# Optimization experiments

Hardware: AMD Instinct MI355X
Metric: run time of the kernel (lower is better)

## Reference

```python
import math
import jax, jax.numpy as jnp
import numpy as np

N_NODES = 100000
N_EDGES = 1200000
N_BASIS = 20
HIDDEN = 50
SILU_NORM = 1.679  # e3nn normalize2mom constant for silu
LMAX_SH = 5
MID_LS = (0, 1, 2, 3, 4)          # middle = 1x0e+1x1o+1x2e+1x3o+1x4e (dim 25)
OUT_L = 2                          # out = 1x2e (dim 5)
TP2_PATHS = ((0, 2), (1, 1), (1, 3), (2, 0), (2, 2), (2, 4), (3, 1), (3, 3), (3, 5), (4, 2), (4, 4))
NUM_NEIGHBORS = 6


def _fact(n):
    return math.factorial(n)


def _cg(j1, m1, j2, m2, j3, m3):
    # Racah formula for Clebsch-Gordan coefficients (complex SH, Condon-Shortley).
    if m1 + m2 != m3:
        return 0.0
    pref = math.sqrt((2 * j3 + 1) * _fact(j1 + j2 - j3) * _fact(j1 - j2 + j3) * _fact(-j1 + j2 + j3) / _fact(j1 + j2 + j3 + 1))
    pref *= math.sqrt(_fact(j1 + m1) * _fact(j1 - m1) * _fact(j2 + m2) * _fact(j2 - m2) * _fact(j3 + m3) * _fact(j3 - m3))
    s = 0.0
    for k in range(j1 + j2 - j3 + 1):
        d = (k, j1 + j2 - j3 - k, j1 - m1 - k, j2 + m2 - k, j3 - j2 + m1 + k, j3 - j1 - m2 + k)
        if min(d) < 0:
            continue
        den = 1.0
        for q in d:
            den *= _fact(q)
        s += (-1.0) ** k / den
    return pref * s


def _u_real(l):
    # change of basis complex SH -> real SH, rows indexed by real m=-l..l
    U = np.zeros((2 * l + 1, 2 * l + 1), dtype=np.complex128)
    U[l, l] = 1.0
    rt2 = math.sqrt(2.0)
    for m in range(1, l + 1):
        U[l + m, l + m] = (-1.0) ** m / rt2
        U[l + m, l - m] = 1.0 / rt2
        U[l - m, l + m] = -1j * (-1.0) ** m / rt2
        U[l - m, l - m] = 1j / rt2
    return U


def _w3j_real(j1, j2, j3):
    # real-basis Wigner 3j tensor (real for even j1+j2+j3, which holds for all paths here)
    Wc = np.zeros((2 * j1 + 1, 2 * j2 + 1, 2 * j3 + 1), dtype=np.complex128)
    for m1 in range(-j1, j1 + 1):
        for m2 in range(-j2, j2 + 1):
            m3 = -(m1 + m2)
            if abs(m3) <= j3:
                Wc[j1 + m1, j2 + m2, j3 + m3] = (-1.0) ** (j1 - j2 - m3) / math.sqrt(2 * j3 + 1) * _cg(j1, m1, j2, m2, j3, -m3)
    U1, U2, U3 = _u_real(j1).conj(), _u_real(j2).conj(), _u_real(j3).conj()
    Wr = np.einsum('abc,ia,jb,kc->ijk', Wc, U1, U2, U3)
    return np.ascontiguousarray(Wr.real.astype(np.float32))


W3J_TP1 = {l: _w3j_real(0, l, l) for l in MID_LS}
W3J_TP2 = {p: _w3j_real(p[0], p[1], OUT_L) for p in TP2_PATHS}


def spherical_harmonics(vec):
    # vec [E,3] -> component-normalized real SH for l=0..5, concatenated [E,36]
    r = jnp.sqrt(jnp.sum(vec * vec, axis=1))
    x, y, z = vec[:, 0] / r, vec[:, 1] / r, vec[:, 2] / r
    phi = jnp.arctan2(y, x)
    s = jnp.sqrt(jnp.clip(1.0 - z * z, 0.0, 1.0))
    # associated Legendre P[l][m] without Condon-Shortley phase
    P = [[None] * (l + 1) for l in range(LMAX_SH + 1)]
    P[0][0] = jnp.ones_like(z)
    for m in range(1, LMAX_SH + 1):
        P[m][m] = (2 * m - 1) * s * P[m - 1][m - 1]
    for m in range(0, LMAX_SH):
        P[m + 1][m] = (2 * m + 1) * z * P[m][m]
    for l in range(2, LMAX_SH + 1):
        for m in range(0, l - 1):
            P[l][m] = ((2 * l - 1) * z * P[l - 1][m] - (l - 1 + m) * P[l - 2][m]) / (l - m)
    blocks = []
    for l in range(LMAX_SH + 1):
        comps = []
        for m in range(-l, l + 1):
            am = abs(m)
            c = math.sqrt((2 * l + 1) * _fact(l - am) / _fact(l + am)) * (math.sqrt(2.0) if m != 0 else 1.0)
            if m < 0:
                ang = jnp.sin(am * phi)
            elif m > 0:
                ang = jnp.cos(am * phi)
            else:
                ang = jnp.ones_like(phi)
            comps.append(c * P[l][am] * ang)
        blocks.append(jnp.stack(comps, axis=1))
    return jnp.concatenate(blocks, axis=1)


def soft_one_hot(d):
    # e3nn soft_one_hot_linspace(basis='smooth_finite', cutoff=True), start=0, end=3
    values = jnp.linspace(0.0, 3.0, N_BASIS + 2)
    step = values[1] - values[0]
    values = values[1:-1]
    diff = (d[:, None] - values[None, :]) / step

    def sus(t):
        safe = jnp.where(t > 0, t, 1.0)
        return jnp.where(t > 0, jnp.exp(-1.0 / safe), 0.0)

    return 1.14136 * math.exp(2.0) * sus(diff + 1.0) * sus(1.0 - diff)


def tp1(x_scalar, sh, w):
    # FullyConnectedTensorProduct(1x0e, sh, middle) with external per-edge weights w [E,5]
    outs = []
    for i, l in enumerate(MID_LS):
        W = W3J_TP1[l][0]                       # [2l+1, 2l+1]
        alpha = math.sqrt(2 * l + 1)            # sqrt(dim_out / fan_in), fan_in = 1
        shl = sh[:, l * l:(l + 1) * (l + 1)]
        outs.append(alpha * w[:, i:i + 1] * x_scalar * (shl @ W))
    return jnp.concatenate(outs, axis=1)        # [E, 25]


def tp2(feat, sh, w):
    # FullyConnectedTensorProduct(middle, sh, 1x2e) with internal weights w [11]
    alpha = math.sqrt((2 * OUT_L + 1) / len(TP2_PATHS))
    out = jnp.zeros((feat.shape[0], 2 * OUT_L + 1), dtype=feat.dtype)
    for p, (l1, l2) in enumerate(TP2_PATHS):
        W = W3J_TP2[(l1, l2)]                   # [2l1+1, 2l2+1, 5]
        f = feat[:, l1 * l1:(l1 + 1) * (l1 + 1)]
        s = sh[:, l2 * l2:(l2 + 1) * (l2 + 1)]
        tmp = jnp.einsum('ei,ijk->ejk', f, W)
        out = out + (alpha * w[p]) * jnp.einsum('ejk,ej->ek', tmp, s)
    return out                                   # [E, 5]


def _forward(x, pos, edge_index, mlp_w1, mlp_w2, tp2_w):
    N = pos.shape[0]
    edge_from = edge_index[:, 0]
    edge_to = edge_index[:, 1]
    Co = jnp.argmax(jnp.bincount(edge_to, length=N))          # torch.mode(edge_to)
    edge_vec = pos[edge_to] - pos[edge_from]
    sh = spherical_harmonics(edge_vec)                         # [E, 36]
    dist = jnp.linalg.norm(edge_vec, axis=1)
    emb = soft_one_hot(dist)                                   # [E, 20]
    h = jax.nn.silu(emb @ mlp_w1 / math.sqrt(N_BASIS)) * SILU_NORM
    tp_w = h @ mlp_w2 / math.sqrt(HIDDEN)                      # [E, 5]
    feat = tp1(x[edge_to], sh, tp_w)                           # [E, 25]
    node = jax.ops.segment_sum(feat, edge_from, num_segments=N) / math.sqrt(float(NUM_NEIGHBORS))
    feat2 = tp2(node[edge_to], sh, tp2_w)                      # [E, 5]
    node2 = jax.ops.segment_sum(feat2, edge_from, num_segments=N)
    return node2[Co]                                           # [5]


def setup_inputs():
    N, E = N_NODES, N_EDGES
    key = jax.random.key(0)
    k = jax.random.split(key, 7)
    pos = 1.5 * jax.random.normal(k[0], (N, 3), dtype=jnp.float32)
    x = jax.random.normal(k[1], (N, 1), dtype=jnp.float32)
    ef = jax.random.randint(k[2], (E,), 0, N, dtype=jnp.int32)
    off = jax.random.randint(k[3], (E,), 1, N, dtype=jnp.int32)
    et = (ef + off) % N                                        # no self loops -> nonzero edge_vec
    edge_index = jnp.stack([ef, et], axis=1)
    mlp_w1 = jax.random.normal(k[4], (N_BASIS, HIDDEN), dtype=jnp.float32)
    mlp_w2 = jax.random.normal(k[5], (HIDDEN, len(MID_LS)), dtype=jnp.float32)
    tp2_w = jax.random.normal(k[6], (len(TP2_PATHS),), dtype=jnp.float32)
    return {'x': x, 'pos': pos, 'edge_index': edge_index, 'mlp_w1': mlp_w1, 'mlp_w2': mlp_w2, 'tp2_w': tp2_w}


def reference(x, pos, edge_index, mlp_w1, mlp_w2, tp2_w):
    return _forward(x, pos, edge_index, mlp_w1, mlp_w2, tp2_w)
```

## Files before the change

kernel.cpp:

```cpp
#include <hip/hip_runtime.h>
#include <math.h>

#define CAP 2048
#define HALF_MAX 12544


struct WSPtrs {
  unsigned* slices;
  int* flag;
  unsigned long long* key;
  int* co_count;
  int* s_count;
  int* co_edges;
  float* node_acc;
  float* w3j1;
  float* w3j2;
  size_t fb_zero_bytes;
  size_t total_bytes;
};

__host__ __device__ inline WSPtrs make_ws(char* ws, int N, int half, int C, int fb){
  WSPtrs p;
  size_t o = 0;
  p.slices   = (unsigned*)(ws + o);
  o += fb ? (size_t)N * 4 : (size_t)C * 2 * half * 4;
  p.flag     = (int*)(ws + o); o += (size_t)N * 4;
  o = (o + 7) & ~(size_t)7;
  p.key      = (unsigned long long*)(ws + o); o += 8;
  p.co_count = (int*)(ws + o); o += 4;
  p.s_count  = (int*)(ws + o); o += 4;
  p.co_edges = (int*)(ws + o); o += (size_t)CAP * 4;
  p.node_acc = (float*)(ws + o); o += (size_t)CAP * 25 * 4;
  p.fb_zero_bytes = o;
  p.w3j1     = (float*)(ws + o); o += 165 * 4;
  p.w3j2     = (float*)(ws + o); o += 1915 * 4;
  p.total_bytes = o;
  return p;
}


__device__ double cg_coef_lut(int j1,int m1,int j2,int m2,int j3,int m3, const double* __restrict__ fact){
  if (m1 + m2 != m3) return 0.0;
  double pref = sqrt((2.0*j3+1.0) * fact[j1+j2-j3] * fact[j1-j2+j3] * fact[-j1+j2+j3]
                     / fact[j1+j2+j3+1]);
  pref *= sqrt(fact[j1+m1]*fact[j1-m1]*fact[j2+m2]*fact[j2-m2]*fact[j3+m3]*fact[j3-m3]);
  double s = 0.0;
  for (int k = 0; k <= j1+j2-j3; ++k){
    int d2 = j1-m1-k, d3 = j2+m2-k, d4 = j3-j2+m1+k, d5 = j3-j1-m2+k;
    if (d2 < 0 || d3 < 0 || d4 < 0 || d5 < 0) continue;
    double den = fact[k]*fact[j1+j2-j3-k]*fact[d2]*fact[d3]*fact[d4]*fact[d5];
    s += ((k & 1) ? -1.0 : 1.0) / den;
  }
  return pref * s;
}

__device__ double wigner_c_val_lut(int j1,int j2,int j3,int m1,int m2,int m3, const double* __restrict__ fact){
  if (m1+m2+m3 != 0) return 0.0;
  int e = j1 - j2 - m3;
  double sign = (e & 1) ? -1.0 : 1.0;
  return sign / sqrt(2.0*j3+1.0) * cg_coef_lut(j1,m1,j2,m2,j3,-m3,fact);
}

__device__ int conjU_row(int l, int i, int* cols, double* re, double* im){
  int mr = i - l;
  const double irt2 = 0.70710678118654752440;
  if (mr == 0){ cols[0]=l; re[0]=1.0; im[0]=0.0; return 1; }
  int m = mr > 0 ? mr : -mr;
  double sgn = (m & 1) ? -1.0 : 1.0;
  if (mr > 0){
    cols[0]=l+m; re[0]=sgn*irt2; im[0]=0.0;
    cols[1]=l-m; re[1]=irt2;     im[1]=0.0;
  } else {
    cols[0]=l+m; re[0]=0.0; im[0]= sgn*irt2;
    cols[1]=l-m; re[1]=0.0; im[1]=-irt2;
  }
  return 2;
}

__device__ void wigner_entry(int entry, const double* __restrict__ sfact,
                             float* __restrict__ w3j1, float* __restrict__ w3j2){
  if (entry >= 165 + 1915) return;
  int j1, j2, j3, ii, jj, kk;
  float* dst;
  if (entry < 165){
    const int l1off[5] = {0,1,10,35,84};
    int l = 4;
    for (int q = 1; q < 5; ++q) if (entry < l1off[q]){ l = q-1; break; }
    int t = entry - l1off[l];
    int n = 2*l+1;
    j1 = 0; j2 = l; j3 = l;
    ii = 0; jj = t / n; kk = t % n;
    dst = &w3j1[entry];
  } else {
    int t2 = entry - 165;
    const int pl1[11]  = {0,1,1,2,2,2,3,3,3,4,4};
    const int pl2[11]  = {2,1,3,0,2,4,1,3,5,2,4};
    const int poff[11] = {0,25,70,175,200,325,550,655,900,1285,1510};
    int p = 10;
    for (int q = 1; q < 11; ++q) if (t2 < poff[q]){ p = q-1; break; }
    int t = t2 - poff[p];
    j1 = pl1[p]; j2 = pl2[p]; j3 = 2;
    int n2q = 2*j2+1;
    ii = t / (n2q*5); int rem = t % (n2q*5); jj = rem / 5; kk = rem % 5;
    dst = &w3j2[t2];
  }
  int c1[2], c2[2], c3[2];
  double r1[2], i1[2], r2[2], i2[2], r3[2], i3[2];
  int n1 = conjU_row(j1, ii, c1, r1, i1);
  int n2 = conjU_row(j2, jj, c2, r2, i2);
  int n3 = conjU_row(j3, kk, c3, r3, i3);
  double acc = 0.0;
  for (int combo = 0; combo < 8; ++combo){
    int a = (combo >> 2) & 1, b = (combo >> 1) & 1, c = combo & 1;
    if (a >= n1 || b >= n2 || c >= n3) continue;
    int m1 = c1[a]-j1, m2 = c2[b]-j2, m3 = c3[c]-j3;
    if (m1 + m2 + m3 != 0) continue;
    double wc = wigner_c_val_lut(j1,j2,j3,m1,m2,m3,sfact);
    if (wc == 0.0) continue;
    double pr = r1[a]*r2[b] - i1[a]*i2[b];
    double pi = r1[a]*i2[b] + i1[a]*r2[b];
    acc += wc * (pr*r3[c] - pi*i3[c]);
  }
  *dst = (float)acc;
}


__device__ void compute_sh36f(float ex, float ey, float ez, float* __restrict__ sh){
  float r = sqrtf(ex*ex + ey*ey + ez*ez);
  float x = ex/r, y = ey/r, z = ez/r;
  float t = 1.0f - z*z;
  t = t < 0.0f ? 0.0f : (t > 1.0f ? 1.0f : t);
  float s = sqrtf(t);
  float rxy = sqrtf(x*x + y*y);
  float c1, s1;
  if (rxy > 1e-30f){ c1 = x/rxy; s1 = y/rxy; } else { c1 = 1.0f; s1 = 0.0f; }
  float cm[6], sm[6];
  cm[0] = 1.0f; sm[0] = 0.0f;
  for (int m = 1; m <= 5; ++m){
    cm[m] = cm[m-1]*c1 - sm[m-1]*s1;
    sm[m] = sm[m-1]*c1 + cm[m-1]*s1;
  }
  float P[6][6];
  P[0][0] = 1.0f;
  for (int m=1;m<=5;m++) P[m][m] = (float)(2*m-1)*s*P[m-1][m-1];
  for (int m=0;m<5;m++)  P[m+1][m] = (float)(2*m+1)*z*P[m][m];
  for (int l=2;l<=5;l++)
    for (int m=0;m<=l-2;m++)
      P[l][m] = ((float)(2*l-1)*z*P[l-1][m] - (float)(l-1+m)*P[l-2][m])/(float)(l-m);
  const float rt2 = 1.41421356237309504880f;
  for (int l=0;l<=5;l++){
    for (int m=-l;m<=l;m++){
      int am = m < 0 ? -m : m;
      float ratio = 1.0f;
      for (int k = l-am+1; k <= l+am; ++k) ratio *= (float)k;
      float c = sqrtf((float)(2*l+1)/ratio);
      if (m != 0) c *= rt2;
      float ang = (m < 0) ? sm[am] : ((m > 0) ? cm[am] : 1.0f);
      sh[l*l + m + l] = c * P[l][am] * ang;
    }
  }
}

__device__ void feat_edge(int f, int t, const int* __restrict__ flag,
                          const float* __restrict__ pos, const float* __restrict__ x,
                          const float* w1, const float* w2,
                          const float* w3j1, float* __restrict__ node_acc){
  int slot = flag[f] - 1;
  if (slot < 0 || slot >= CAP) return;

  float ex = pos[3*t+0] - pos[3*f+0];
  float ey = pos[3*t+1] - pos[3*f+1];
  float ez = pos[3*t+2] - pos[3*f+2];
  float sh[36];
  compute_sh36f(ex,ey,ez,sh);
  float d = sqrtf(ex*ex+ey*ey+ez*ez);

  float emb[20];
  const float step = 3.0f/21.0f;
  const float cemb = 1.14136f * 7.38905609893065f;
  for (int jb=0;jb<20;jb++){
    float v = step*(float)(jb+1);
    float diff = (d - v)/step;
    float a = diff + 1.0f, b = 1.0f - diff;
    float sa = (a > 0.0f) ? __expf(-1.0f/a) : 0.0f;
    float sb = (b > 0.0f) ? __expf(-1.0f/b) : 0.0f;
    emb[jb] = cemb * sa * sb;
  }
  float tw[5] = {0,0,0,0,0};
  const float is20 = 0.22360679774997896964f;
  const float is50 = 0.14142135623730950488f;
  for (int kk=0;kk<50;kk++){
    float z = 0.0f;
    for (int jb=0;jb<20;jb++) z += emb[jb]*w1[jb*50+kk];
    z *= is20;
    float hk = (z / (1.0f + __expf(-z))) * 1.679f;
    for (int i=0;i<5;i++) tw[i] += hk * w2[kk*5+i];
  }
  for (int i=0;i<5;i++) tw[i] *= is50;

  float xs = x[t];
  const int w1off[5] = {0,1,10,35,84};
  const float alphal[5] = {1.0f, 1.73205080756887729353f, 2.23606797749978969641f,
                           2.64575131106459059050f, 3.0f};
  int fo = 0;
  for (int l=0;l<5;l++){
    int nl = 2*l+1;
    float scale = alphal[l] * tw[l] * xs;
    for (int kq=0;kq<nl;kq++){
      float acc = 0.0f;
      for (int jq=0;jq<nl;jq++) acc += sh[l*l+jq]*w3j1[w1off[l]+jq*nl+kq];
      atomicAdd(&node_acc[slot*25 + fo + kq], scale*acc);
    }
    fo += nl;
  }
}

__device__ void tp2_task(int e, int p, const int2* __restrict__ ei, const int* __restrict__ flag,
                         const float* __restrict__ pos, const float* __restrict__ node_acc,
                         const float* w3j2, const float* __restrict__ tp2w,
                         float* __restrict__ acc){
  const float inv_sqrt6 = 0.40824829046386301637f;
  const float alpha2    = 0.67419986246324704794f;
  const int pl1[11]  = {0,1,1,2,2,2,3,3,3,4,4};
  const int pl2[11]  = {2,1,3,0,2,4,1,3,5,2,4};
  const int poff[11] = {0,25,70,175,200,325,550,655,900,1285,1510};
  int2 fe = ei[e];
  int f = fe.x, t = fe.y;
  int slot = flag[t] - 1;
  if (slot < 0 || slot >= CAP) return;
  float ex = pos[3*t+0] - pos[3*f+0];
  float ey = pos[3*t+1] - pos[3*f+1];
  float ez = pos[3*t+2] - pos[3*f+2];
  float sh[36];
  compute_sh36f(ex,ey,ez,sh);
  int l1 = pl1[p], l2 = pl2[p], n1 = 2*l1+1, n2 = 2*l2+1;
  const float* W = w3j2 + poff[p];
  float wp = alpha2 * tp2w[p];
  for (int i=0;i<n1;i++){
    float fi = node_acc[slot*25 + l1*l1 + i] * inv_sqrt6;
    for (int j=0;j<n2;j++){
      float fs = wp*fi*sh[l2*l2+j];
      const float* Wij = W + (i*n2+j)*5;
      for (int k=0;k<5;k++) acc[k] += fs*Wij[k];
    }
  }
}


__global__ __launch_bounds__(1024)
void count_w3j_kernel(const int2* __restrict__ ei, unsigned* __restrict__ slices,
                      int* __restrict__ flag, unsigned long long* __restrict__ key,
                      int* __restrict__ co_count, int* __restrict__ s_count,
                      float* __restrict__ node_acc,
                      float* __restrict__ w3j1, float* __restrict__ w3j2,
                      int N, int half, int E, int C){
  __shared__ double sfact[16];
  __shared__ unsigned hist[HALF_MAX];
  if (threadIdx.x == 0){
    double rr = 1.0;
    sfact[0] = 1.0;
    for (int i = 1; i < 16; ++i){ rr *= (double)i; sfact[i] = rr; }
  }
  for (int i = threadIdx.x; i < half; i += blockDim.x) hist[i] = 0;
  __syncthreads();

  int gtid = blockIdx.x*blockDim.x + threadIdx.x;
  int gsize = gridDim.x*blockDim.x;

  if (gtid < 2080) wigner_entry(gtid, sfact, w3j1, w3j2);
  for (int i = gtid; i < N; i += gsize) flag[i] = 0;
  for (int i = gtid; i < CAP*25; i += gsize) node_acc[i] = 0.0f;
  if (gtid == 0){ *key = 0ull; *co_count = 0; *s_count = 0; }

  int c = blockIdx.x >> 1;
  int r = blockIdx.x & 1;
  int wbase = r * half;
  size_t e0 = (size_t)c * (size_t)E / (size_t)C;
  size_t e1 = (size_t)(c+1) * (size_t)E / (size_t)C;
  for (size_t e = e0 + threadIdx.x; e < e1; e += blockDim.x){
    int v = ei[e].y;
    int lw = (v >> 2) - wbase;
    if (lw >= 0 && lw < half)
      atomicAdd(&hist[lw], 1u << ((v & 3) * 8));
  }
  __syncthreads();

  unsigned* dst = slices + (size_t)(c*2 + r) * half;
  for (int i = threadIdx.x; i < half; i += blockDim.x) dst[i] = hist[i];
}

__global__ void count_fb_kernel(const int2* __restrict__ ei, unsigned* __restrict__ counts,
                                float* __restrict__ w3j1, float* __restrict__ w3j2, int E){
  __shared__ double sfact[16];
  if (threadIdx.x == 0){
    double rr = 1.0;
    sfact[0] = 1.0;
    for (int i = 1; i < 16; ++i){ rr *= (double)i; sfact[i] = rr; }
  }
  __syncthreads();
  int tid = blockIdx.x*blockDim.x + threadIdx.x;
  if (tid < 2080) wigner_entry(tid, sfact, w3j1, w3j2);
  if (tid < E) atomicAdd(&counts[ei[tid].y], 1u);
}

__global__ void argmax_kernel(const unsigned* __restrict__ slices, unsigned long long* __restrict__ key,
                              int N, int Nw, int half, int C, int fb){
  __shared__ unsigned long long sred[256];
  int w = blockIdx.x*blockDim.x + threadIdx.x;
  unsigned long long best = 0;
  if (fb){
    if (w < N)
      best = ((unsigned long long)slices[w] << 32) | (unsigned)(N-1-w);
  } else if (w < Nw){
    int r = (w >= half) ? 1 : 0;
    int lw = w - r*half;
    unsigned sum = 0;
    for (int c = 0; c < C; ++c)
      sum += slices[(size_t)(c*2 + r) * half + lw];
    for (int q = 0; q < 4; ++q){
      int idx = w*4 + q;
      if (idx < N){
        unsigned cnt = (sum >> (q*8)) & 0xffu;
        unsigned long long k = ((unsigned long long)cnt << 32) | (unsigned)(N-1-idx);
        if (k > best) best = k;
      }
    }
  }
  sred[threadIdx.x] = best;
  __syncthreads();
  for (int s = 128; s > 0; s >>= 1){
    if (threadIdx.x < s){
      unsigned long long o = sred[threadIdx.x+s];
      if (o > sred[threadIdx.x]) sred[threadIdx.x] = o;
    }
    __syncthreads();
  }
  if (threadIdx.x == 0) atomicMax(key, sred[0]);
}

__global__ void find_co_kernel(const int2* __restrict__ ei, const unsigned long long* __restrict__ key,
                               int* __restrict__ flag, int* __restrict__ co_count,
                               int* __restrict__ s_count, int* __restrict__ co_edges, int N, int E){
  int e = blockIdx.x*blockDim.x + threadIdx.x;
  if (e >= E) return;
  int Co = N - 1 - (int)(unsigned int)(*key & 0xffffffffull);
  int2 fe = ei[e];
  if (fe.x != Co) return;
  int p = atomicAdd(co_count, 1);
  if (p < CAP) co_edges[p] = e;
  int v = fe.y;
  if (atomicCAS(&flag[v], 0, -1) == 0){
    int slot = atomicAdd(s_count, 1);
    flag[v] = (slot < CAP) ? (slot + 1) : 0;
  }
}

__global__ void collect_feat_kernel(const int2* __restrict__ ei, const int* __restrict__ flag,
                                    const float* __restrict__ pos, const float* __restrict__ x,
                                    const float* __restrict__ w1g, const float* __restrict__ w2g,
                                    const float* __restrict__ w3j1g, float* __restrict__ node_acc,
                                    int E){
  __shared__ float sw1[1000];
  __shared__ float sw2[250];
  __shared__ float sw3j1[165];
  int e = blockIdx.x*blockDim.x + threadIdx.x;
  int2 fe = make_int2(0, 0);
  int has = 0;
  if (e < E){ fe = ei[e]; has = (flag[fe.x] > 0); }
  if (__syncthreads_or(has) == 0) return;

  for (int i = threadIdx.x; i < 1000; i += blockDim.x) sw1[i] = w1g[i];
  for (int i = threadIdx.x; i < 250;  i += blockDim.x) sw2[i] = w2g[i];
  for (int i = threadIdx.x; i < 165;  i += blockDim.x) sw3j1[i] = w3j1g[i];
  __syncthreads();
  if (!has) return;

  feat_edge(fe.x, fe.y, flag, pos, x, sw1, sw2, sw3j1, node_acc);
}

__global__ void out_kernel(const int2* __restrict__ ei, const int* __restrict__ flag,
                           const float* __restrict__ pos, const float* __restrict__ node_acc,
                           const float* __restrict__ w3j2g, const float* __restrict__ tp2w,
                           const int* __restrict__ co_count, const int* __restrict__ co_edges,
                           float* __restrict__ out){
  __shared__ float sw3j2[1915];
  __shared__ float red[256*5];
  for (int i = threadIdx.x; i < 1915; i += blockDim.x) sw3j2[i] = w3j2g[i];
  __syncthreads();
  float acc[5] = {0,0,0,0,0};
  int n = *co_count; if (n > CAP) n = CAP;
  int tasks = n * 11;
  for (int task = threadIdx.x; task < tasks; task += blockDim.x)
    tp2_task(co_edges[task/11], task%11, ei, flag, pos, node_acc, sw3j2, tp2w, acc);
  for (int k=0;k<5;k++) red[threadIdx.x*5+k] = acc[k];
  __syncthreads();
  if (threadIdx.x < 5){
    float s = 0.0f;
    for (int t2=0;t2<256;t2++) s += red[t2*5+threadIdx.x];
    out[threadIdx.x] = s;
  }
}


extern "C" void kernel_launch(void* const* d_in, const int* in_sizes, int n_in,
                              void* d_out, int out_size, void* d_ws, size_t ws_size,
                              hipStream_t stream){
  const int2*  ei2  = (const int2*)d_in[2];
  const float* xp   = (const float*)d_in[0];
  const float* posp = (const float*)d_in[1];
  const float* w1p  = (const float*)d_in[3];
  const float* w2p  = (const float*)d_in[4];
  const float* tpwp = (const float*)d_in[5];
  float* outp = (float*)d_out;
  char* wsp = (char*)d_ws;
  int N = in_sizes[0];
  int E = in_sizes[2] / 2;
  int Nw = (N + 3) >> 2;
  int half = (Nw + 1) >> 1;

  int fb = (half > HALF_MAX) ? 1 : 0;
  int C = 0;
  if (!fb){
    for (int cand = 128; cand >= 8; cand >>= 1){
      WSPtrs p = make_ws(wsp, N, half, cand, 0);
      if (p.total_bytes + 64 <= ws_size){ C = cand; break; }
    }
    if (C == 0) fb = 1;
  }
  WSPtrs P = make_ws(wsp, N, half, fb ? 1 : C, fb);

  int eblocks = (E + 255)/256;
  if (fb){
    hipMemsetAsync(d_ws, 0, P.fb_zero_bytes, stream);
    count_fb_kernel<<<eblocks, 256, 0, stream>>>(ei2, P.slices, P.w3j1, P.w3j2, E);
  } else {
    count_w3j_kernel<<<2*C, 1024, 0, stream>>>(ei2, P.slices, P.flag, P.key,
                                               P.co_count, P.s_count, P.node_acc,
                                               P.w3j1, P.w3j2, N, half, E, C);
  }
  int ablocks = fb ? (N + 255)/256 : (Nw + 255)/256;
  argmax_kernel     <<<ablocks, 256, 0, stream>>>(P.slices, P.key, N, Nw, half, C, fb);
  find_co_kernel    <<<eblocks, 256, 0, stream>>>(ei2, P.key, P.flag, P.co_count, P.s_count,
                                                  P.co_edges, N, E);
  collect_feat_kernel<<<eblocks, 256, 0, stream>>>(ei2, P.flag, posp, xp, w1p, w2p, P.w3j1,
                                                   P.node_acc, E);
  out_kernel        <<<1, 256, 0, stream>>>(ei2, P.flag, posp, P.node_acc, P.w3j2, tpwp,
                                            P.co_count, P.co_edges, outp);
}
```

Measured before the change: 166.7 us.

## Fuse argmax, center search, feature collect and output into one cooperative kernel

Measured after the change: 322.7 us. +93.6%, slower.

```diff
diff --git a/kernel.cpp b/kernel.cpp
--- a/kernel.cpp
+++ b/kernel.cpp
@@ -1,7 +1,11 @@
 #include <hip/hip_runtime.h>
+#include <hip/hip_cooperative_groups.h>
 #include <math.h>
 
+namespace cg = cooperative_groups;
+
 #define CAP 2048
+#define SLIST 64
 #define HALF_MAX 12544
 
 
@@ -11,6 +15,7 @@
   unsigned long long* key;
   int* co_count;
   int* s_count;
+  int* s_nodes;
   int* co_edges;
   float* node_acc;
   float* w3j1;
@@ -29,6 +34,7 @@
   p.key      = (unsigned long long*)(ws + o); o += 8;
   p.co_count = (int*)(ws + o); o += 4;
   p.s_count  = (int*)(ws + o); o += 4;
+  p.s_nodes  = (int*)(ws + o); o += SLIST * 4;
   p.co_edges = (int*)(ws + o); o += (size_t)CAP * 4;
   p.node_acc = (float*)(ws + o); o += (size_t)CAP * 25 * 4;
   p.fb_zero_bytes = o;
@@ -161,13 +167,11 @@
   }
 }
 
-__device__ void feat_edge(int f, int t, const int* __restrict__ flag,
-                          const float* __restrict__ pos, const float* __restrict__ x,
-                          const float* w1, const float* w2,
-                          const float* w3j1, float* __restrict__ node_acc){
-  int slot = flag[f] - 1;
+__device__ void feat_edge_slot(int f, int t, int slot,
+                               const float* __restrict__ pos, const float* __restrict__ x,
+                               const float* w1, const float* w2,
+                               const float* w3j1, float* __restrict__ node_acc){
   if (slot < 0 || slot >= CAP) return;
-
   float ex = pos[3*t+0] - pos[3*f+0];
   float ey = pos[3*t+1] - pos[3*f+1];
   float ez = pos[3*t+2] - pos[3*f+2];
@@ -303,6 +307,124 @@
   if (tid < E) atomicAdd(&counts[ei[tid].y], 1u);
 }
 
+
+__global__ void tail_kernel(const int2* __restrict__ ei, const float* __restrict__ pos,
+                            const float* __restrict__ x, const float* __restrict__ w1g,
+                            const float* __restrict__ w2g, const float* __restrict__ tp2w,
+                            char* __restrict__ ws, float* __restrict__ out,
+                            int N, int Nw, int half, int E, int C, int fb){
+  cg::grid_group grid = cg::this_grid();
+  WSPtrs P = make_ws(ws, N, half, fb ? 1 : C, fb);
+
+  __shared__ unsigned long long sred[256];
+  __shared__ float fred[256*5];
+  __shared__ float sw1[1000];
+  __shared__ float sw2[250];
+  __shared__ float sw3j1[165];
+  __shared__ float sw3j2[1915];
+  __shared__ int s_list[SLIST];
+
+  int tid = blockIdx.x*blockDim.x + threadIdx.x;
+  int nth = gridDim.x*blockDim.x;
+
+  {
+    unsigned long long best = 0;
+    if (fb){
+      const unsigned* counts = P.slices;
+      for (int i = tid; i < N; i += nth){
+        unsigned long long k = ((unsigned long long)counts[i] << 32) | (unsigned)(N-1-i);
+        if (k > best) best = k;
+      }
+    } else {
+      for (int w = tid; w < Nw; w += nth){
+        int r = (w >= half) ? 1 : 0;
+        int lw = w - r*half;
+        unsigned sum = 0;
+        for (int c = 0; c < C; ++c)
+          sum += P.slices[(size_t)(c*2 + r) * half + lw];
+        for (int q = 0; q < 4; ++q){
+          int idx = w*4 + q;
+          if (idx < N){
+            unsigned cnt = (sum >> (q*8)) & 0xffu;
+            unsigned long long k = ((unsigned long long)cnt << 32) | (unsigned)(N-1-idx);
+            if (k > best) best = k;
+          }
+        }
+      }
+    }
+    sred[threadIdx.x] = best;
+    __syncthreads();
+    for (int s = 128; s > 0; s >>= 1){
+      if (threadIdx.x < s){
+        unsigned long long o = sred[threadIdx.x+s];
+        if (o > sred[threadIdx.x]) sred[threadIdx.x] = o;
+      }
+      __syncthreads();
+    }
+    if (threadIdx.x == 0) atomicMax(P.key, sred[0]);
+  }
+  grid.sync();
+
+  {
+    int Co = N - 1 - (int)(unsigned int)(*P.key & 0xffffffffull);
+    for (int e = tid; e < E; e += nth){
+      int2 fe = ei[e];
+      if (fe.x != Co) continue;
+      int p = atomicAdd(P.co_count, 1);
+      if (p < CAP) P.co_edges[p] = e;
+      int v = fe.y;
+      if (atomicCAS(&P.flag[v], 0, -1) == 0){
+        int slot = atomicAdd(P.s_count, 1);
+        P.flag[v] = (slot < CAP) ? (slot + 1) : 0;
+        if (slot < SLIST) P.s_nodes[slot] = v;
+      }
+    }
+  }
+  grid.sync();
+
+  {
+    int nS = *P.s_count;
+    int fastS = (nS <= SLIST) ? nS : 0;
+    for (int i = threadIdx.x; i < 1000; i += blockDim.x) sw1[i] = w1g[i];
+    for (int i = threadIdx.x; i < 250;  i += blockDim.x) sw2[i] = w2g[i];
+    for (int i = threadIdx.x; i < 165;  i += blockDim.x) sw3j1[i] = P.w3j1[i];
+    for (int i = threadIdx.x; i < fastS; i += blockDim.x) s_list[i] = P.s_nodes[i];
+    __syncthreads();
+    for (int e = tid; e < E; e += nth){
+      int2 fe = ei[e];
+      int slot = -1;
+      if (fastS){
+        for (int k = 0; k < fastS; ++k)
+          if (s_list[k] == fe.x){ slot = k; break; }
+      } else {
+        slot = P.flag[fe.x] - 1;
+      }
+      if (slot >= 0)
+        feat_edge_slot(fe.x, fe.y, slot, pos, x, sw1, sw2, sw3j1, P.node_acc);
+    }
+  }
+  grid.sync();
+
+  if (blockIdx.x != 0) return;
+  {
+    for (int i = threadIdx.x; i < 1915; i += blockDim.x) sw3j2[i] = P.w3j2[i];
+    __syncthreads();
+    float acc[5] = {0,0,0,0,0};
+    int n = *P.co_count; if (n > CAP) n = CAP;
+    int tasks = n * 11;
+    for (int task = threadIdx.x; task < tasks; task += blockDim.x)
+      tp2_task(P.co_edges[task/11], task%11, ei, P.flag, pos, P.node_acc, sw3j2, tp2w, acc);
+    for (int k=0;k<5;k++) fred[threadIdx.x*5+k] = acc[k];
+    __syncthreads();
+    if (threadIdx.x < 5){
+      float s = 0.0f;
+      for (int t2=0;t2<256;t2++) s += fred[t2*5+threadIdx.x];
+      out[threadIdx.x] = s;
+    }
+  }
+}
+
+
 __global__ void argmax_kernel(const unsigned* __restrict__ slices, unsigned long long* __restrict__ key,
                               int N, int Nw, int half, int C, int fb){
   __shared__ unsigned long long sred[256];
@@ -365,17 +487,15 @@
   __shared__ float sw3j1[165];
   int e = blockIdx.x*blockDim.x + threadIdx.x;
   int2 fe = make_int2(0, 0);
-  int has = 0;
-  if (e < E){ fe = ei[e]; has = (flag[fe.x] > 0); }
-  if (__syncthreads_or(has) == 0) return;
-
+  int slot = -1;
+  if (e < E){ fe = ei[e]; slot = flag[fe.x] - 1; }
+  if (__syncthreads_or(slot >= 0) == 0) return;
   for (int i = threadIdx.x; i < 1000; i += blockDim.x) sw1[i] = w1g[i];
   for (int i = threadIdx.x; i < 250;  i += blockDim.x) sw2[i] = w2g[i];
   for (int i = threadIdx.x; i < 165;  i += blockDim.x) sw3j1[i] = w3j1g[i];
   __syncthreads();
-  if (!has) return;
-
-  feat_edge(fe.x, fe.y, flag, pos, x, sw1, sw2, sw3j1, node_acc);
+  if (slot >= 0)
+    feat_edge_slot(fe.x, fe.y, slot, pos, x, sw1, sw2, sw3j1, node_acc);
 }
 
 __global__ void out_kernel(const int2* __restrict__ ei, const int* __restrict__ flag,
@@ -438,12 +558,27 @@
                                                P.co_count, P.s_count, P.node_acc,
                                                P.w3j1, P.w3j2, N, half, E, C);
   }
-  int ablocks = fb ? (N + 255)/256 : (Nw + 255)/256;
-  argmax_kernel     <<<ablocks, 256, 0, stream>>>(P.slices, P.key, N, Nw, half, C, fb);
-  find_co_kernel    <<<eblocks, 256, 0, stream>>>(ei2, P.key, P.flag, P.co_count, P.s_count,
-                                                  P.co_edges, N, E);
-  collect_feat_kernel<<<eblocks, 256, 0, stream>>>(ei2, P.flag, posp, xp, w1p, w2p, P.w3j1,
-                                                   P.node_acc, E);
-  out_kernel        <<<1, 256, 0, stream>>>(ei2, P.flag, posp, P.node_acc, P.w3j2, tpwp,
-                                            P.co_count, P.co_edges, outp);
-}
+
+  bool coop = false;
+  int occ = 0;
+  if (hipOccupancyMaxActiveBlocksPerMultiprocessor(&occ, (const void*)tail_kernel, 256, 0)
+      == hipSuccess && occ > 0){
+    int tblocks = 256;
+    void* args[] = {(void*)&ei2, (void*)&posp, (void*)&xp, (void*)&w1p, (void*)&w2p,
+                    (void*)&tpwp, (void*)&wsp, (void*)&outp,
+                    (void*)&N, (void*)&Nw, (void*)&half, (void*)&E, (void*)&C, (void*)&fb};
+    coop = (hipLaunchCooperativeKernel((const void*)tail_kernel, dim3(tblocks), dim3(256),
+                                       args, 0, stream) == hipSuccess);
+  }
+  if (!coop){
+    (void)hipGetLastError();
+    int ablocks = fb ? (N + 255)/256 : (Nw + 255)/256;
+    argmax_kernel      <<<ablocks, 256, 0, stream>>>(P.slices, P.key, N, Nw, half, C, fb);
+    find_co_kernel     <<<eblocks, 256, 0, stream>>>(ei2, P.key, P.flag, P.co_count, P.s_count,
+                                                     P.co_edges, N, E);
+    collect_feat_kernel<<<eblocks, 256, 0, stream>>>(ei2, P.flag, posp, xp, w1p, w2p, P.w3j1,
+                                                     P.node_acc, E);
+    out_kernel         <<<1, 256, 0, stream>>>(ei2, P.flag, posp, P.node_acc, P.w3j2, tpwp,
+                                               P.co_count, P.co_edges, outp);
+  }
+}
```
